# Kernel tuning notes

Measured on AMD Instinct MI355X. Metric: run time of the kernel, lower is better.

The kernel has to match this reference:

```python
import jax, jax.numpy as jnp
import numpy as np

N_NODES = 100_000
N_EDGES = 1_600_000
HIDDEN = 128
NUM_RBF = 64
NUM_FILTERS = 128
CUTOFF_UPPER = 5.0


def _xavier(key, fan_in, fan_out):
    limit = np.sqrt(6.0 / (fan_in + fan_out)).astype(np.float32)
    return jax.random.uniform(key, (fan_in, fan_out), jnp.float32, -limit, limit)


def setup_inputs() -> dict:
    key = jax.random.key(0)
    ks = jax.random.split(key, 10)
    x = jax.random.normal(ks[0], (N_NODES, HIDDEN), jnp.float32)
    edge_index = jax.random.randint(ks[1], (2, N_EDGES), 0, N_NODES, jnp.int64)
    # distances in [0, cutoff_upper)
    edge_weight = jax.random.uniform(ks[2], (N_EDGES,), jnp.float32) * CUTOFF_UPPER
    edge_attr = jax.random.normal(ks[3], (N_EDGES, NUM_RBF), jnp.float32)
    return {
        "x": x,
        "edge_index": edge_index,
        "edge_weight": edge_weight,
        "edge_attr": edge_attr,
        "mlp_w1": _xavier(ks[4], NUM_RBF, NUM_FILTERS),
        "mlp_b1": jnp.zeros((NUM_FILTERS,), jnp.float32),
        "mlp_w2": _xavier(ks[5], NUM_FILTERS, NUM_FILTERS),
        "mlp_b2": jnp.zeros((NUM_FILTERS,), jnp.float32),
        "lin1_w": _xavier(ks[6], HIDDEN, NUM_FILTERS),   # no bias
        "lin2_w": _xavier(ks[7], NUM_FILTERS, HIDDEN),
        "lin2_b": jnp.zeros((HIDDEN,), jnp.float32),
        "lin_w": _xavier(ks[8], HIDDEN, HIDDEN),
        "lin_b": jnp.zeros((HIDDEN,), jnp.float32),
    }


def reference(x, edge_index, edge_weight, edge_attr,
              mlp_w1, mlp_b1, mlp_w2, mlp_b2,
              lin1_w, lin2_w, lin2_b, lin_w, lin_b):
    n_nodes = x.shape[0]
    src, dst = edge_index[0], edge_index[1]

    # cosine cutoff (cutoff_lower == 0 branch)
    C = 0.5 * (jnp.cos(edge_weight * (jnp.pi / CUTOFF_UPPER)) + 1.0)
    C = C * (edge_weight < CUTOFF_UPPER).astype(x.dtype)

    # edge filter: MLP(edge_attr) * C   -> [E, F]
    h = jax.nn.silu(edge_attr @ mlp_w1 + mlp_b1)
    W = (h @ mlp_w2 + mlp_b2) * C[:, None]

    # CFConv: lin1 -> gather * W -> scatter-mean -> lin2
    xf = x @ lin1_w                       # [N, F]
    msg = xf[src] * W                     # [E, F]
    agg_sum = jax.ops.segment_sum(msg, dst, num_segments=n_nodes)
    cnt = jax.ops.segment_sum(jnp.ones((msg.shape[0],), x.dtype), dst,
                              num_segments=n_nodes)
    agg = agg_sum / jnp.maximum(cnt, 1.0)[:, None]
    out = agg @ lin2_w + lin2_b

    # interaction block tail: act -> lin
    out = jax.nn.silu(out)
    out = out @ lin_w + lin_b
    return out
```

## Files before the change

kernel.cpp:

```cpp
#include <hip/hip_runtime.h>
#include <hip/hip_bf16.h>

#define HIDDEN 128
#define NRBF 64

typedef __attribute__((ext_vector_type(8))) short short8;
typedef __attribute__((ext_vector_type(4))) float float4v;

#define ATTR_LD 72
#define H_LD 136
#define MSG_LD 132

static __device__ __forceinline__ float silu(float v) {
    return v / (1.0f + __expf(-v));
}

static __device__ __forceinline__ short f2bf(float v) {
    __hip_bfloat16 b = __float2bfloat16(v);
    return *reinterpret_cast<short*>(&b);
}

__global__ __launch_bounds__(256) void conv_weights(
    const float* __restrict__ w1, const float* __restrict__ w2,
    short* __restrict__ w1f, short* __restrict__ w2f) {
    int idx = blockIdx.x * 256 + threadIdx.x;
    if (idx < HIDDEN * NRBF) {
        int n = idx >> 6, k = idx & 63;
        w1f[idx] = f2bf(w1[k * HIDDEN + n]);
    }
    if (idx < HIDDEN * HIDDEN) {
        int n = idx >> 7, k = idx & 127;
        w2f[idx] = f2bf(w2[k * HIDDEN + n]);
    }
}

__global__ __launch_bounds__(256) void gemm32(
    const float* __restrict__ in, const float* __restrict__ w,
    float* __restrict__ out, int N) {
    __shared__ float rows[32][HIDDEN];
    const int n0 = blockIdx.x * 32;
    const int tid = threadIdx.x;

    const float4* ag = (const float4*)(in + (size_t)n0 * HIDDEN);
    float4 v[4];
#pragma unroll
    for (int i = 0; i < 4; ++i) {
        int fi = i * 256 + tid;
        int nr = n0 + (fi >> 5);
        v[i] = (nr < N) ? ag[fi] : make_float4(0.f, 0.f, 0.f, 0.f);
    }
#pragma unroll
    for (int i = 0; i < 4; ++i) {
        int fi = i * 256 + tid;
        ((float4*)rows)[fi] = v[i];
    }
    __syncthreads();

    const int f = tid & 127;
    const int ng = tid >> 7;
    float acc[16];
#pragma unroll
    for (int j = 0; j < 16; ++j) acc[j] = 0.0f;

    for (int k4 = 0; k4 < HIDDEN / 4; ++k4) {
        const float* wp = w + k4 * 4 * HIDDEN + f;
        float w0 = wp[0], w1 = wp[HIDDEN], w2 = wp[2 * HIDDEN], w3 = wp[3 * HIDDEN];
#pragma unroll
        for (int j = 0; j < 16; ++j) {
            float4 r = *(const float4*)&rows[ng * 16 + j][k4 * 4];
            acc[j] += r.x * w0 + r.y * w1 + r.z * w2 + r.w * w3;
        }
    }
#pragma unroll
    for (int j = 0; j < 16; ++j) {
        int n = n0 + ng * 16 + j;
        if (n < N) out[(size_t)n * HIDDEN + f] = acc[j];
    }
}

__global__ void hist_kernel(const int* __restrict__ dst, int* __restrict__ counts, int E) {
    int e = blockIdx.x * 256 + threadIdx.x;
    if (e < E) atomicAdd(&counts[dst[e]], 1);
}

__global__ __launch_bounds__(256) void scan_part1(
    const int* __restrict__ counts, int* __restrict__ bsums, int n) {
    int base = blockIdx.x * 1024;
    int t = threadIdx.x;
    int s = 0;
#pragma unroll
    for (int j = 0; j < 4; ++j) {
        int i = base + t * 4 + j;
        if (i < n) s += counts[i];
    }
    for (int off = 32; off; off >>= 1) s += __shfl_down(s, off, 64);
    __shared__ int wsum[4];
    if ((t & 63) == 0) wsum[t >> 6] = s;
    __syncthreads();
    if (t == 0) bsums[blockIdx.x] = wsum[0] + wsum[1] + wsum[2] + wsum[3];
}

__global__ __launch_bounds__(1024) void scan_part2(
    int* __restrict__ bsums, int nb, int* __restrict__ off_total) {
    __shared__ int sd[1024];
    int t = threadIdx.x;
    int v = (t < nb) ? bsums[t] : 0;
    sd[t] = v;
    __syncthreads();
    for (int s = 1; s < 1024; s <<= 1) {
        int u = (t >= s) ? sd[t - s] : 0;
        __syncthreads();
        sd[t] += u;
        __syncthreads();
    }
    if (t < nb) bsums[t] = sd[t] - v;
    if (t == 1023) *off_total = sd[1023];
}

__global__ __launch_bounds__(256) void scan_part3(
    const int* __restrict__ counts, const int* __restrict__ bsums,
    int* __restrict__ off, int* __restrict__ cursor, int n) {
    int base = blockIdx.x * 1024;
    int t = threadIdx.x;
    int i0 = base + t * 4;
    int v[4];
#pragma unroll
    for (int j = 0; j < 4; ++j) v[j] = (i0 + j < n) ? counts[i0 + j] : 0;
    int tsum = v[0] + v[1] + v[2] + v[3];
    int incl = tsum;
    for (int d = 1; d < 64; d <<= 1) {
        int u = __shfl_up(incl, d, 64);
        if ((t & 63) >= d) incl += u;
    }
    __shared__ int wtot[4];
    if ((t & 63) == 63) wtot[t >> 6] = incl;
    __syncthreads();
    int woff = 0;
    for (int w = 0; w < (t >> 6); ++w) woff += wtot[w];
    int run = bsums[blockIdx.x] + woff + (incl - tsum);
#pragma unroll
    for (int j = 0; j < 4; ++j) {
        if (i0 + j < n) {
            off[i0 + j] = run;
            cursor[i0 + j] = run;
            run += v[j];
        }
    }
}

__global__ void fill_kernel(const int* __restrict__ dst, int* __restrict__ cursor,
                            int* __restrict__ csr, int E) {
    int e = blockIdx.x * 256 + threadIdx.x;
    if (e < E) {
        int pos = atomicAdd(&cursor[dst[e]], 1);
        csr[pos] = e;
    }
}

__global__ __launch_bounds__(256, 4) void msg_mfma(
    const int* __restrict__ csr, const int* __restrict__ src,
    const int* __restrict__ dstp,
    const float* __restrict__ ew, const float* __restrict__ attr,
    const short* __restrict__ w1f, const float* __restrict__ b1,
    const short* __restrict__ w2f, const float* __restrict__ b2,
    const float* __restrict__ xf, float* __restrict__ agg, int E) {
    __shared__ __align__(16) short uni[128 * H_LD];
    short* attr_s = uni;
    short* h_s    = uni;
    short* msg_s  = uni;
    __shared__ int srcs[128];
    __shared__ int dstn[128];
    __shared__ float Cc[128];

    const int p0 = blockIdx.x * 128;
    const int tid = threadIdx.x;
    const int wave = tid >> 6;
    const int lane = tid & 63;
    const int quad = lane >> 4;
    const int lc = lane & 15;
    const int nbase = wave * 32;

    {
        int row = tid >> 1;
        int half = tid & 1;
        int p = p0 + row;
        int eid = (p < E) ? csr[p] : 0;
        if (half == 0) {
            srcs[row] = src[eid];
            dstn[row] = (p < E) ? dstp[eid] : -1;
            float w = ew[eid];
            float C = 0.5f * (__cosf(w * 0.62831853071795865f) + 1.0f);
            if (w >= 5.0f) C = 0.0f;
            Cc[row] = C;
        }
        const float4* ap = (const float4*)(attr + (size_t)eid * NRBF + half * 32);
        short* dp = attr_s + row * ATTR_LD + half * 32;
#pragma unroll
        for (int i = 0; i < 8; ++i) {
            float4 v = ap[i];
            short4 s4;
            s4.x = f2bf(v.x); s4.y = f2bf(v.y); s4.z = f2bf(v.z); s4.w = f2bf(v.w);
            *(short4*)(dp + i * 4) = s4;
        }
    }
    __syncthreads();

    float4v acc[8][2];
#pragma unroll
    for (int mt = 0; mt < 8; ++mt)
#pragma unroll
        for (int nt = 0; nt < 2; ++nt) acc[mt][nt] = (float4v){0.f, 0.f, 0.f, 0.f};

    short8 bf1[2][2];
#pragma unroll
    for (int kk = 0; kk < 2; ++kk)
#pragma unroll
        for (int nt = 0; nt < 2; ++nt)
            bf1[kk][nt] = *(const short8*)(w1f + (nbase + nt * 16 + lc) * NRBF + kk * 32 + quad * 8);

#pragma unroll
    for (int kk = 0; kk < 2; ++kk) {
#pragma unroll
        for (int mt = 0; mt < 8; ++mt) {
            short8 af = *(const short8*)(attr_s + (mt * 16 + lc) * ATTR_LD + kk * 32 + quad * 8);
            acc[mt][0] = __builtin_amdgcn_mfma_f32_16x16x32_bf16(af, bf1[kk][0], acc[mt][0], 0, 0, 0);
            acc[mt][1] = __builtin_amdgcn_mfma_f32_16x16x32_bf16(af, bf1[kk][1], acc[mt][1], 0, 0, 0);
        }
    }
    __syncthreads();

#pragma unroll
    for (int nt = 0; nt < 2; ++nt) {
        int col = nbase + nt * 16 + lc;
        float bb = b1[col];
#pragma unroll
        for (int mt = 0; mt < 8; ++mt) {
            float4v a = acc[mt][nt];
#pragma unroll
            for (int r = 0; r < 4; ++r) {
                int row = mt * 16 + quad * 4 + r;
                h_s[row * H_LD + col] = f2bf(silu(a[r] + bb));
            }
        }
    }
    __syncthreads();

    float4v acc2[8][2];
#pragma unroll
    for (int mt = 0; mt < 8; ++mt)
#pragma unroll
        for (int nt = 0; nt < 2; ++nt) acc2[mt][nt] = (float4v){0.f, 0.f, 0.f, 0.f};

#pragma unroll
    for (int kk = 0; kk < 4; ++kk) {
        short8 bb0 = *(const short8*)(w2f + (nbase + 0 * 16 + lc) * HIDDEN + kk * 32 + quad * 8);
        short8 bb1 = *(const short8*)(w2f + (nbase + 1 * 16 + lc) * HIDDEN + kk * 32 + quad * 8);
#pragma unroll
        for (int mt = 0; mt < 8; ++mt) {
            short8 af = *(const short8*)(h_s + (mt * 16 + lc) * H_LD + kk * 32 + quad * 8);
            acc2[mt][0] = __builtin_amdgcn_mfma_f32_16x16x32_bf16(af, bb0, acc2[mt][0], 0, 0, 0);
            acc2[mt][1] = __builtin_amdgcn_mfma_f32_16x16x32_bf16(af, bb1, acc2[mt][1], 0, 0, 0);
        }
    }

#pragma unroll
    for (int nt = 0; nt < 2; ++nt) {
        int f = nbase + nt * 16 + lc;
        float bb = b2[f];
#pragma unroll
        for (int mt = 0; mt < 8; ++mt) {
#pragma unroll
            for (int r = 0; r < 4; ++r) {
                int row = mt * 16 + quad * 4 + r;
                int p = p0 + row;
                float v = 0.0f;
                if (p < E) {
                    float Wv = (acc2[mt][nt][r] + bb) * Cc[row];
                    float xv = xf[(size_t)srcs[row] * HIDDEN + f];
                    v = xv * Wv;
                }
                acc2[mt][nt][r] = v;
            }
        }
    }
    __syncthreads();

#pragma unroll
    for (int nt = 0; nt < 2; ++nt) {
        int f = nbase + nt * 16 + lc;
#pragma unroll
        for (int mt = 0; mt < 8; ++mt) {
#pragma unroll
            for (int r = 0; r < 4; ++r) {
                int row = mt * 16 + quad * 4 + r;
                msg_s[row * MSG_LD + f] = f2bf(acc2[mt][nt][r]);
            }
        }
    }
    __syncthreads();

    {
        int f = tid & 127;
        int half = tid >> 7;
        int r0 = half * 64;
        float s = 0.0f;
        int cur = dstn[r0];
        for (int r = r0; r < r0 + 64; ++r) {
            int d = dstn[r];
            if (d != cur) {
                if (cur >= 0) atomicAdd(&agg[(size_t)cur * HIDDEN + f], s);
                s = 0.0f;
                cur = d;
            }
            s += __bfloat162float(*(const __hip_bfloat16*)&msg_s[r * MSG_LD + f]);
        }
        if (cur >= 0) atomicAdd(&agg[(size_t)cur * HIDDEN + f], s);
    }
}

__global__ __launch_bounds__(256) void tail32(
    const int* __restrict__ off, const float* __restrict__ agg,
    const float* __restrict__ l2w, const float* __restrict__ l2b,
    const float* __restrict__ lw, const float* __restrict__ lb,
    float* __restrict__ out, int N) {
    __shared__ float rows[32][HIDDEN];
    __shared__ float dinv[32];
    const int n0 = blockIdx.x * 32;
    const int tid = threadIdx.x;

    if (tid < 32) {
        int n = n0 + tid;
        float d = 1.0f;
        if (n < N) d = fmaxf((float)(off[n + 1] - off[n]), 1.0f);
        dinv[tid] = 1.0f / d;
    }

    const float4* ag = (const float4*)(agg + (size_t)n0 * HIDDEN);
    float4 v[4];
#pragma unroll
    for (int i = 0; i < 4; ++i) {
        int fi = i * 256 + tid;
        int nr = n0 + (fi >> 5);
        v[i] = (nr < N) ? ag[fi] : make_float4(0.f, 0.f, 0.f, 0.f);
    }
    __syncthreads();
#pragma unroll
    for (int i = 0; i < 4; ++i) {
        int fi = i * 256 + tid;
        float s = dinv[fi >> 5];
        float4 r;
        r.x = v[i].x * s; r.y = v[i].y * s; r.z = v[i].z * s; r.w = v[i].w * s;
        ((float4*)rows)[fi] = r;
    }
    __syncthreads();

    const int f = tid & 127;
    const int ng = tid >> 7;

    float acc[16];
    {
        float bb = l2b[f];
#pragma unroll
        for (int j = 0; j < 16; ++j) acc[j] = bb;
    }
    for (int k4 = 0; k4 < HIDDEN / 4; ++k4) {
        const float* wp = l2w + k4 * 4 * HIDDEN + f;
        float w0 = wp[0], w1 = wp[HIDDEN], w2 = wp[2 * HIDDEN], w3 = wp[3 * HIDDEN];
#pragma unroll
        for (int j = 0; j < 16; ++j) {
            float4 r = *(const float4*)&rows[ng * 16 + j][k4 * 4];
            acc[j] += r.x * w0 + r.y * w1 + r.z * w2 + r.w * w3;
        }
    }
#pragma unroll
    for (int j = 0; j < 16; ++j) acc[j] = silu(acc[j]);
    __syncthreads();
#pragma unroll
    for (int j = 0; j < 16; ++j) rows[ng * 16 + j][f] = acc[j];
    __syncthreads();

    float acc2[16];
    {
        float bb = lb[f];
#pragma unroll
        for (int j = 0; j < 16; ++j) acc2[j] = bb;
    }
    for (int k4 = 0; k4 < HIDDEN / 4; ++k4) {
        const float* wp = lw + k4 * 4 * HIDDEN + f;
        float w0 = wp[0], w1 = wp[HIDDEN], w2 = wp[2 * HIDDEN], w3 = wp[3 * HIDDEN];
#pragma unroll
        for (int j = 0; j < 16; ++j) {
            float4 r = *(const float4*)&rows[ng * 16 + j][k4 * 4];
            acc2[j] += r.x * w0 + r.y * w1 + r.z * w2 + r.w * w3;
        }
    }
#pragma unroll
    for (int j = 0; j < 16; ++j) {
        int n = n0 + ng * 16 + j;
        if (n < N) out[(size_t)n * HIDDEN + f] = acc2[j];
    }
}

static inline char* align_up(char* p, size_t a) {
    return (char*)(((uintptr_t)p + a - 1) & ~(uintptr_t)(a - 1));
}

extern "C" void kernel_launch(void* const* d_in, const int* in_sizes, int n_in,
                              void* d_out, int out_size, void* d_ws, size_t ws_size,
                              hipStream_t stream) {
    const float* x   = (const float*)d_in[0];
    const int*   ei  = (const int*)d_in[1];
    const float* ew  = (const float*)d_in[2];
    const float* ea  = (const float*)d_in[3];
    const float* w1  = (const float*)d_in[4];
    const float* b1  = (const float*)d_in[5];
    const float* w2  = (const float*)d_in[6];
    const float* b2  = (const float*)d_in[7];
    const float* l1w = (const float*)d_in[8];
    const float* l2w = (const float*)d_in[9];
    const float* l2b = (const float*)d_in[10];
    const float* lw  = (const float*)d_in[11];
    const float* lb  = (const float*)d_in[12];

    const int N = in_sizes[0] / HIDDEN;
    const int E = in_sizes[2];
    const int* src = ei;
    const int* dst = ei + E;

    const int NB = (N + 1023) / 1024;

    char* p = (char*)d_ws;
    float* xf = (float*)p;        p = align_up(p + (size_t)N * HIDDEN * 4, 256);
    short* w1f = (short*)p;       p = align_up(p + HIDDEN * NRBF * 2, 256);
    short* w2f = (short*)p;       p = align_up(p + HIDDEN * HIDDEN * 2, 256);
    int* counts = (int*)p;        p = align_up(p + (size_t)N * 4, 256);
    int* off = (int*)p;           p = align_up(p + (size_t)(N + 1) * 4, 256);
    int* cursor = (int*)p;        p = align_up(p + (size_t)N * 4, 256);
    int* bsums = (int*)p;         p = align_up(p + (size_t)NB * 4, 256);
    int* csr = (int*)p;           p = align_up(p + (size_t)E * 4, 256);
    float* agg = (float*)p;

    hipMemsetAsync(counts, 0, (size_t)N * sizeof(int), stream);
    hipMemsetAsync(agg, 0, (size_t)N * HIDDEN * sizeof(float), stream);

    conv_weights<<<(HIDDEN * HIDDEN + 255) / 256, 256, 0, stream>>>(w1, w2, w1f, w2f);

    gemm32<<<(N + 31) / 32, 256, 0, stream>>>(x, l1w, xf, N);

    hist_kernel<<<(E + 255) / 256, 256, 0, stream>>>(dst, counts, E);
    scan_part1<<<NB, 256, 0, stream>>>(counts, bsums, N);
    scan_part2<<<1, 1024, 0, stream>>>(bsums, NB, off + N);
    scan_part3<<<NB, 256, 0, stream>>>(counts, bsums, off, cursor, N);
    fill_kernel<<<(E + 255) / 256, 256, 0, stream>>>(dst, cursor, csr, E);

    msg_mfma<<<(E + 127) / 128, 256, 0, stream>>>(
        csr, src, dst, ew, ea, w1f, b1, w2f, b2, xf, agg, E);

    tail32<<<(N + 31) / 32, 256, 0, stream>>>(
        off, agg, l2w, l2b, lw, lb, (float*)d_out, N);
}
```

Baseline: 1.488 ms.

## Shrink edge tile, drop shared staging in node GEMMs, split tail kernel

The message kernel now processes 64 edges per block instead of 128. That halves LDS use and accumulator registers and raises the launch-bounds occupancy hint from 4 to 7. The node GEMMs (lin1 and both tail linears) no longer stage rows in shared memory. They read rows straight from global with wave-uniform addresses through readfirstlane. The fused tail is split into two kernels that pass the SiLU activation through a reused workspace buffer, which adds a global round trip. Smaller edge tiles also mean more blocks and more atomics for segments that cross block boundaries.

Result: slower. 1.645 ms (+10.6%).

```diff
diff --git a/kernel.cpp b/kernel.cpp
--- a/kernel.cpp
+++ b/kernel.cpp
@@ -34,30 +34,15 @@
     }
 }
 
-__global__ __launch_bounds__(256) void gemm32(
+__global__ __launch_bounds__(256) void xf_gemm(
     const float* __restrict__ in, const float* __restrict__ w,
     float* __restrict__ out, int N) {
-    __shared__ float rows[32][HIDDEN];
     const int n0 = blockIdx.x * 32;
     const int tid = threadIdx.x;
-
-    const float4* ag = (const float4*)(in + (size_t)n0 * HIDDEN);
-    float4 v[4];
-#pragma unroll
-    for (int i = 0; i < 4; ++i) {
-        int fi = i * 256 + tid;
-        int nr = n0 + (fi >> 5);
-        v[i] = (nr < N) ? ag[fi] : make_float4(0.f, 0.f, 0.f, 0.f);
-    }
-#pragma unroll
-    for (int i = 0; i < 4; ++i) {
-        int fi = i * 256 + tid;
-        ((float4*)rows)[fi] = v[i];
-    }
-    __syncthreads();
-
     const int f = tid & 127;
     const int ng = tid >> 7;
+    const int r0 = n0 + ng * 16;
+
     float acc[16];
 #pragma unroll
     for (int j = 0; j < 16; ++j) acc[j] = 0.0f;
@@ -67,14 +52,87 @@
         float w0 = wp[0], w1 = wp[HIDDEN], w2 = wp[2 * HIDDEN], w3 = wp[3 * HIDDEN];
 #pragma unroll
         for (int j = 0; j < 16; ++j) {
-            float4 r = *(const float4*)&rows[ng * 16 + j][k4 * 4];
+            int rr = r0 + j;
+            if (rr >= N) rr = N - 1;
+            rr = __builtin_amdgcn_readfirstlane(rr);
+            float4 r = *(const float4*)(in + (size_t)rr * HIDDEN + k4 * 4);
             acc[j] += r.x * w0 + r.y * w1 + r.z * w2 + r.w * w3;
         }
     }
 #pragma unroll
     for (int j = 0; j < 16; ++j) {
-        int n = n0 + ng * 16 + j;
+        int n = r0 + j;
         if (n < N) out[(size_t)n * HIDDEN + f] = acc[j];
+    }
+}
+
+__global__ __launch_bounds__(256) void tail_a(
+    const int* __restrict__ off, const float* __restrict__ agg,
+    const float* __restrict__ w, const float* __restrict__ b,
+    float* __restrict__ act, int N) {
+    const int n0 = blockIdx.x * 32;
+    const int tid = threadIdx.x;
+    const int f = tid & 127;
+    const int ng = tid >> 7;
+    const int r0 = n0 + ng * 16;
+
+    float acc[16];
+#pragma unroll
+    for (int j = 0; j < 16; ++j) acc[j] = 0.0f;
+
+    for (int k4 = 0; k4 < HIDDEN / 4; ++k4) {
+        const float* wp = w + k4 * 4 * HIDDEN + f;
+        float w0 = wp[0], w1 = wp[HIDDEN], w2 = wp[2 * HIDDEN], w3 = wp[3 * HIDDEN];
+#pragma unroll
+        for (int j = 0; j < 16; ++j) {
+            int rr = r0 + j;
+            if (rr >= N) rr = N - 1;
+            rr = __builtin_amdgcn_readfirstlane(rr);
+            float4 r = *(const float4*)(agg + (size_t)rr * HIDDEN + k4 * 4);
+            acc[j] += r.x * w0 + r.y * w1 + r.z * w2 + r.w * w3;
+        }
+    }
+    float bb = b[f];
+#pragma unroll
+    for (int j = 0; j < 16; ++j) {
+        int n = r0 + j;
+        if (n < N) {
+            float di = 1.0f / fmaxf((float)(off[n + 1] - off[n]), 1.0f);
+            act[(size_t)n * HIDDEN + f] = silu(acc[j] * di + bb);
+        }
+    }
+}
+
+__global__ __launch_bounds__(256) void tail_b(
+    const float* __restrict__ act, const float* __restrict__ w,
+    const float* __restrict__ b, float* __restrict__ out, int N) {
+    const int n0 = blockIdx.x * 32;
+    const int tid = threadIdx.x;
+    const int f = tid & 127;
+    const int ng = tid >> 7;
+    const int r0 = n0 + ng * 16;
+
+    float acc[16];
+#pragma unroll
+    for (int j = 0; j < 16; ++j) acc[j] = 0.0f;
+
+    for (int k4 = 0; k4 < HIDDEN / 4; ++k4) {
+        const float* wp = w + k4 * 4 * HIDDEN + f;
+        float w0 = wp[0], w1 = wp[HIDDEN], w2 = wp[2 * HIDDEN], w3 = wp[3 * HIDDEN];
+#pragma unroll
+        for (int j = 0; j < 16; ++j) {
+            int rr = r0 + j;
+            if (rr >= N) rr = N - 1;
+            rr = __builtin_amdgcn_readfirstlane(rr);
+            float4 r = *(const float4*)(act + (size_t)rr * HIDDEN + k4 * 4);
+            acc[j] += r.x * w0 + r.y * w1 + r.z * w2 + r.w * w3;
+        }
+    }
+    float bb = b[f];
+#pragma unroll
+    for (int j = 0; j < 16; ++j) {
+        int n = r0 + j;
+        if (n < N) out[(size_t)n * HIDDEN + f] = acc[j] + bb;
     }
 }
 
@@ -157,22 +215,22 @@
     }
 }
 
-__global__ __launch_bounds__(256, 4) void msg_mfma(
+__global__ __launch_bounds__(256, 7) void msg_mfma(
     const int* __restrict__ csr, const int* __restrict__ src,
     const int* __restrict__ dstp,
     const float* __restrict__ ew, const float* __restrict__ attr,
     const short* __restrict__ w1f, const float* __restrict__ b1,
     const short* __restrict__ w2f, const float* __restrict__ b2,
     const float* __restrict__ xf, float* __restrict__ agg, int E) {
-    __shared__ __align__(16) short uni[128 * H_LD];
+    __shared__ __align__(16) short uni[64 * H_LD];
     short* attr_s = uni;
     short* h_s    = uni;
     short* msg_s  = uni;
-    __shared__ int srcs[128];
-    __shared__ int dstn[128];
-    __shared__ float Cc[128];
-
-    const int p0 = blockIdx.x * 128;
+    __shared__ int srcs[64];
+    __shared__ int dstn[64];
+    __shared__ float Cc[64];
+
+    const int p0 = blockIdx.x * 64;
     const int tid = threadIdx.x;
     const int wave = tid >> 6;
     const int lane = tid & 63;
@@ -181,11 +239,11 @@
     const int nbase = wave * 32;
 
     {
-        int row = tid >> 1;
-        int half = tid & 1;
+        int row = tid >> 2;
+        int part = tid & 3;
         int p = p0 + row;
         int eid = (p < E) ? csr[p] : 0;
-        if (half == 0) {
+        if (part == 0) {
             srcs[row] = src[eid];
             dstn[row] = (p < E) ? dstp[eid] : -1;
             float w = ew[eid];
@@ -193,10 +251,10 @@
             if (w >= 5.0f) C = 0.0f;
             Cc[row] = C;
         }
-        const float4* ap = (const float4*)(attr + (size_t)eid * NRBF + half * 32);
-        short* dp = attr_s + row * ATTR_LD + half * 32;
-#pragma unroll
-        for (int i = 0; i < 8; ++i) {
+        const float4* ap = (const float4*)(attr + (size_t)eid * NRBF + part * 16);
+        short* dp = attr_s + row * ATTR_LD + part * 16;
+#pragma unroll
+        for (int i = 0; i < 4; ++i) {
             float4 v = ap[i];
             short4 s4;
             s4.x = f2bf(v.x); s4.y = f2bf(v.y); s4.z = f2bf(v.z); s4.w = f2bf(v.w);
@@ -205,26 +263,21 @@
     }
     __syncthreads();
 
-    float4v acc[8][2];
-#pragma unroll
-    for (int mt = 0; mt < 8; ++mt)
+    float4v acc[4][2];
+#pragma unroll
+    for (int mt = 0; mt < 4; ++mt)
 #pragma unroll
         for (int nt = 0; nt < 2; ++nt) acc[mt][nt] = (float4v){0.f, 0.f, 0.f, 0.f};
 
-    short8 bf1[2][2];
-#pragma unroll
-    for (int kk = 0; kk < 2; ++kk)
-#pragma unroll
-        for (int nt = 0; nt < 2; ++nt)
-            bf1[kk][nt] = *(const short8*)(w1f + (nbase + nt * 16 + lc) * NRBF + kk * 32 + quad * 8);
-
 #pragma unroll
     for (int kk = 0; kk < 2; ++kk) {
-#pragma unroll
-        for (int mt = 0; mt < 8; ++mt) {
+        short8 b0 = *(const short8*)(w1f + (nbase + 0 * 16 + lc) * NRBF + kk * 32 + quad * 8);
+        short8 b1v = *(const short8*)(w1f + (nbase + 1 * 16 + lc) * NRBF + kk * 32 + quad * 8);
+#pragma unroll
+        for (int mt = 0; mt < 4; ++mt) {
             short8 af = *(const short8*)(attr_s + (mt * 16 + lc) * ATTR_LD + kk * 32 + quad * 8);
-            acc[mt][0] = __builtin_amdgcn_mfma_f32_16x16x32_bf16(af, bf1[kk][0], acc[mt][0], 0, 0, 0);
-            acc[mt][1] = __builtin_amdgcn_mfma_f32_16x16x32_bf16(af, bf1[kk][1], acc[mt][1], 0, 0, 0);
+            acc[mt][0] = __builtin_amdgcn_mfma_f32_16x16x32_bf16(af, b0, acc[mt][0], 0, 0, 0);
+            acc[mt][1] = __builtin_amdgcn_mfma_f32_16x16x32_bf16(af, b1v, acc[mt][1], 0, 0, 0);
         }
     }
     __syncthreads();
@@ -234,7 +287,7 @@
         int col = nbase + nt * 16 + lc;
         float bb = b1[col];
 #pragma unroll
-        for (int mt = 0; mt < 8; ++mt) {
+        for (int mt = 0; mt < 4; ++mt) {
             float4v a = acc[mt][nt];
 #pragma unroll
             for (int r = 0; r < 4; ++r) {
@@ -245,9 +298,9 @@
     }
     __syncthreads();
 
-    float4v acc2[8][2];
-#pragma unroll
-    for (int mt = 0; mt < 8; ++mt)
+    float4v acc2[4][2];
+#pragma unroll
+    for (int mt = 0; mt < 4; ++mt)
 #pragma unroll
         for (int nt = 0; nt < 2; ++nt) acc2[mt][nt] = (float4v){0.f, 0.f, 0.f, 0.f};
 
@@ -256,7 +309,7 @@
         short8 bb0 = *(const short8*)(w2f + (nbase + 0 * 16 + lc) * HIDDEN + kk * 32 + quad * 8);
         short8 bb1 = *(const short8*)(w2f + (nbase + 1 * 16 + lc) * HIDDEN + kk * 32 + quad * 8);
 #pragma unroll
-        for (int mt = 0; mt < 8; ++mt) {
+        for (int mt = 0; mt < 4; ++mt) {
             short8 af = *(const short8*)(h_s + (mt * 16 + lc) * H_LD + kk * 32 + quad * 8);
             acc2[mt][0] = __builtin_amdgcn_mfma_f32_16x16x32_bf16(af, bb0, acc2[mt][0], 0, 0, 0);
             acc2[mt][1] = __builtin_amdgcn_mfma_f32_16x16x32_bf16(af, bb1, acc2[mt][1], 0, 0, 0);
@@ -268,7 +321,7 @@
         int f = nbase + nt * 16 + lc;
         float bb = b2[f];
 #pragma unroll
-        for (int mt = 0; mt < 8; ++mt) {
+        for (int mt = 0; mt < 4; ++mt) {
 #pragma unroll
             for (int r = 0; r < 4; ++r) {
                 int row = mt * 16 + quad * 4 + r;
@@ -289,7 +342,7 @@
     for (int nt = 0; nt < 2; ++nt) {
         int f = nbase + nt * 16 + lc;
 #pragma unroll
-        for (int mt = 0; mt < 8; ++mt) {
+        for (int mt = 0; mt < 4; ++mt) {
 #pragma unroll
             for (int r = 0; r < 4; ++r) {
                 int row = mt * 16 + quad * 4 + r;
@@ -302,10 +355,10 @@
     {
         int f = tid & 127;
         int half = tid >> 7;
-        int r0 = half * 64;
+        int r0 = half * 32;
         float s = 0.0f;
         int cur = dstn[r0];
-        for (int r = r0; r < r0 + 64; ++r) {
+        for (int r = r0; r < r0 + 32; ++r) {
             int d = dstn[r];
             if (d != cur) {
                 if (cur >= 0) atomicAdd(&agg[(size_t)cur * HIDDEN + f], s);
@@ -315,89 +368,6 @@
             s += __bfloat162float(*(const __hip_bfloat16*)&msg_s[r * MSG_LD + f]);
         }
         if (cur >= 0) atomicAdd(&agg[(size_t)cur * HIDDEN + f], s);
-    }
-}
-
-__global__ __launch_bounds__(256) void tail32(
-    const int* __restrict__ off, const float* __restrict__ agg,
-    const float* __restrict__ l2w, const float* __restrict__ l2b,
-    const float* __restrict__ lw, const float* __restrict__ lb,
-    float* __restrict__ out, int N) {
-    __shared__ float rows[32][HIDDEN];
-    __shared__ float dinv[32];
-    const int n0 = blockIdx.x * 32;
-    const int tid = threadIdx.x;
-
-    if (tid < 32) {
-        int n = n0 + tid;
-        float d = 1.0f;
-        if (n < N) d = fmaxf((float)(off[n + 1] - off[n]), 1.0f);
-        dinv[tid] = 1.0f / d;
-    }
-
-    const float4* ag = (const float4*)(agg + (size_t)n0 * HIDDEN);
-    float4 v[4];
-#pragma unroll
-    for (int i = 0; i < 4; ++i) {
-        int fi = i * 256 + tid;
-        int nr = n0 + (fi >> 5);
-        v[i] = (nr < N) ? ag[fi] : make_float4(0.f, 0.f, 0.f, 0.f);
-    }
-    __syncthreads();
-#pragma unroll
-    for (int i = 0; i < 4; ++i) {
-        int fi = i * 256 + tid;
-        float s = dinv[fi >> 5];
-        float4 r;
-        r.x = v[i].x * s; r.y = v[i].y * s; r.z = v[i].z * s; r.w = v[i].w * s;
-        ((float4*)rows)[fi] = r;
-    }
-    __syncthreads();
-
-    const int f = tid & 127;
-    const int ng = tid >> 7;
-
-    float acc[16];
-    {
-        float bb = l2b[f];
-#pragma unroll
-        for (int j = 0; j < 16; ++j) acc[j] = bb;
-    }
-    for (int k4 = 0; k4 < HIDDEN / 4; ++k4) {
-        const float* wp = l2w + k4 * 4 * HIDDEN + f;
-        float w0 = wp[0], w1 = wp[HIDDEN], w2 = wp[2 * HIDDEN], w3 = wp[3 * HIDDEN];
-#pragma unroll
-        for (int j = 0; j < 16; ++j) {
-            float4 r = *(const float4*)&rows[ng * 16 + j][k4 * 4];
-            acc[j] += r.x * w0 + r.y * w1 + r.z * w2 + r.w * w3;
-        }
-    }
-#pragma unroll
-    for (int j = 0; j < 16; ++j) acc[j] = silu(acc[j]);
-    __syncthreads();
-#pragma unroll
-    for (int j = 0; j < 16; ++j) rows[ng * 16 + j][f] = acc[j];
-    __syncthreads();
-
-    float acc2[16];
-    {
-        float bb = lb[f];
-#pragma unroll
-        for (int j = 0; j < 16; ++j) acc2[j] = bb;
-    }
-    for (int k4 = 0; k4 < HIDDEN / 4; ++k4) {
-        const float* wp = lw + k4 * 4 * HIDDEN + f;
-        float w0 = wp[0], w1 = wp[HIDDEN], w2 = wp[2 * HIDDEN], w3 = wp[3 * HIDDEN];
-#pragma unroll
-        for (int j = 0; j < 16; ++j) {
-            float4 r = *(const float4*)&rows[ng * 16 + j][k4 * 4];
-            acc2[j] += r.x * w0 + r.y * w1 + r.z * w2 + r.w * w3;
-        }
-    }
-#pragma unroll
-    for (int j = 0; j < 16; ++j) {
-        int n = n0 + ng * 16 + j;
-        if (n < N) out[(size_t)n * HIDDEN + f] = acc2[j];
     }
 }
 
@@ -439,13 +409,14 @@
     int* bsums = (int*)p;         p = align_up(p + (size_t)NB * 4, 256);
     int* csr = (int*)p;           p = align_up(p + (size_t)E * 4, 256);
     float* agg = (float*)p;
+    float* act = xf;
 
     hipMemsetAsync(counts, 0, (size_t)N * sizeof(int), stream);
     hipMemsetAsync(agg, 0, (size_t)N * HIDDEN * sizeof(float), stream);
 
     conv_weights<<<(HIDDEN * HIDDEN + 255) / 256, 256, 0, stream>>>(w1, w2, w1f, w2f);
 
-    gemm32<<<(N + 31) / 32, 256, 0, stream>>>(x, l1w, xf, N);
+    xf_gemm<<<(N + 31) / 32, 256, 0, stream>>>(x, l1w, xf, N);
 
     hist_kernel<<<(E + 255) / 256, 256, 0, stream>>>(dst, counts, E);
     scan_part1<<<NB, 256, 0, stream>>>(counts, bsums, N);
@@ -453,9 +424,9 @@
     scan_part3<<<NB, 256, 0, stream>>>(counts, bsums, off, cursor, N);
     fill_kernel<<<(E + 255) / 256, 256, 0, stream>>>(dst, cursor, csr, E);
 
-    msg_mfma<<<(E + 127) / 128, 256, 0, stream>>>(
+    msg_mfma<<<(E + 63) / 64, 256, 0, stream>>>(
         csr, src, dst, ew, ea, w1f, b1, w2f, b2, xf, agg, E);
 
-    tail32<<<(N + 31) / 32, 256, 0, stream>>>(
-        off, agg, l2w, l2b, lw, lb, (float*)d_out, N);
-}
+    tail_a<<<(N + 31) / 32, 256, 0, stream>>>(off, agg, l2w, l2b, act, N);
+    tail_b<<<(N + 31) / 32, 256, 0, stream>>>(act, lw, lb, (float*)d_out, N);
+}
```
